# Kernel tuning notes

Hardware: AMD Instinct MI355X
Metric: run time of the kernel (lower is better)

## Reference

```python
import jax, jax.numpy as jnp
import numpy as np

TAU = 1.0
EPS_LN = 1e-5


def setup_inputs() -> dict:
    key = jax.random.key(0)
    ks = jax.random.split(key, 6)
    B, D, C, E, H = 32768, 768, 474, 3, 128
    x = jax.random.normal(ks[0], (B, D), dtype=jnp.float32)
    # pre-sampled uniform -> gumbel noise happens in reference; here store standard
    # gumbel noise directly (equivalent distribution to -log(-log(U)))
    u = jax.random.uniform(ks[1], (B, E), dtype=jnp.float32)
    gumbel_noise = -jnp.log(-jnp.log(u + 1e-20) + 1e-20)
    sel_w1 = jax.random.normal(ks[2], (D, H), dtype=jnp.float32) * (1.0 / np.sqrt(D))
    sel_b1 = jnp.zeros((H,), dtype=jnp.float32)
    sel_w2 = jax.random.normal(ks[3], (H, E), dtype=jnp.float32) * (1.0 / np.sqrt(H))
    sel_b2 = jnp.zeros((E,), dtype=jnp.float32)
    ln_gamma = jnp.ones((E, D), dtype=jnp.float32)
    ln_beta = jnp.zeros((E, D), dtype=jnp.float32)
    head_w = jax.random.normal(ks[4], (E, D, C), dtype=jnp.float32) * (1.0 / np.sqrt(D))
    head_b = jnp.zeros((E, C), dtype=jnp.float32)
    return {"x": x, "gumbel_noise": gumbel_noise, "sel_w1": sel_w1, "sel_b1": sel_b1,
            "sel_w2": sel_w2, "sel_b2": sel_b2, "ln_gamma": ln_gamma, "ln_beta": ln_beta,
            "head_w": head_w, "head_b": head_b}


def reference(x, gumbel_noise, sel_w1, sel_b1, sel_w2, sel_b2,
              ln_gamma, ln_beta, head_w, head_b):
    # selector MLP: Linear(768,128) -> ReLU -> Linear(128,3)
    h = jax.nn.relu(x @ sel_w1 + sel_b1)
    logits = h @ sel_w2 + sel_b2                       # [B, 3]

    # hard gumbel-softmax with straight-through estimator
    y = jax.nn.softmax((logits + gumbel_noise) / TAU, axis=-1)
    y_hard = jax.nn.one_hot(jnp.argmax(y, axis=-1), y.shape[-1], dtype=y.dtype)
    selection = jax.lax.stop_gradient(y_hard - y) + y  # [B, 3]

    # 3 expert heads: LayerNorm(768) -> Linear(768,474); dropout is identity (eval)
    mu = jnp.mean(x, axis=-1, keepdims=True)
    var = jnp.mean((x - mu) ** 2, axis=-1, keepdims=True)
    xn = (x - mu) * jax.lax.rsqrt(var + EPS_LN)        # [B, D]
    xs = xn[:, None, :] * ln_gamma[None] + ln_beta[None]   # [B, 3, D]
    outputs = jnp.einsum('bed,edc->bec', xs, head_w) + head_b  # [B, 3, C]

    # mask-and-sum combine
    return jnp.sum(outputs * selection[:, :, None], axis=1)    # [B, C]
```

## Files before the change

### kernel.cpp

```cpp
#include <hip/hip_runtime.h>
#include <hip/hip_bf16.h>
#include <math.h>

#define NB 32768
#define ND 768
#define NC 474
#define NCP 512
#define NE 3
#define NH 128
#define GAP_THR 0.035f
#define XB_OFF 4194304ull

typedef short v8s __attribute__((ext_vector_type(8)));
typedef float v4f __attribute__((ext_vector_type(4)));
typedef unsigned long long u64;

#define GLD16(gp, lp) __builtin_amdgcn_global_load_lds( \
    (const __attribute__((address_space(1))) void*)(gp), \
    (__attribute__((address_space(3))) void*)(lp), 16, 0, 0)

static __device__ __forceinline__ short f2bf(float f) {
    __hip_bfloat16 h = __float2bfloat16(f);
    return *reinterpret_cast<short*>(&h);
}

static __device__ __forceinline__ void vmwait(int n) {
    switch (n) {
    case 0:  asm volatile("s_waitcnt vmcnt(0)"  ::: "memory"); break;
    case 3:  asm volatile("s_waitcnt vmcnt(3)"  ::: "memory"); break;
    case 6:  asm volatile("s_waitcnt vmcnt(6)"  ::: "memory"); break;
    default: asm volatile("s_waitcnt vmcnt(10)" ::: "memory"); break;
    }
}

__global__ __launch_bounds__(256) void ln_convert(
    const float* __restrict__ x, float2* __restrict__ murs,
    short* __restrict__ xb)
{
    const int t = threadIdx.x;
    const int row = blockIdx.x * 16 + (t >> 4);
    const int q = t & 15;
    const float* xr = x + (size_t)row * ND;
    short* xo = xb + (size_t)row * ND;
    float4 v[12];
    #pragma unroll
    for (int i = 0; i < 12; ++i)
        v[i] = *(const float4*)(xr + (i * 16 + q) * 4);
    float s1 = 0.f, s2 = 0.f;
    #pragma unroll
    for (int i = 0; i < 12; ++i) {
        s1 += v[i].x + v[i].y + v[i].z + v[i].w;
        s2 += v[i].x*v[i].x + v[i].y*v[i].y + v[i].z*v[i].z + v[i].w*v[i].w;
    }
    #pragma unroll
    for (int i = 0; i < 12; ++i) {
        short4 o;
        o.x = f2bf(v[i].x); o.y = f2bf(v[i].y);
        o.z = f2bf(v[i].z); o.w = f2bf(v[i].w);
        *(short4*)(xo + (i * 16 + q) * 4) = o;
    }
    s1 += __shfl_xor(s1, 1); s2 += __shfl_xor(s2, 1);
    s1 += __shfl_xor(s1, 2); s2 += __shfl_xor(s2, 2);
    s1 += __shfl_xor(s1, 4); s2 += __shfl_xor(s2, 4);
    s1 += __shfl_xor(s1, 8); s2 += __shfl_xor(s2, 8);
    if (q == 0) {
        const float mu = s1 * (1.f / 768.f);
        const float var = s2 * (1.f / 768.f) - mu * mu;
        murs[row] = make_float2(mu, rsqrtf(var + 1e-5f));
    }
}

__global__ __launch_bounds__(256) void prep_kernel(
    const float* __restrict__ hw, const float* __restrict__ gamma,
    const float* __restrict__ beta, const float* __restrict__ w1,
    const float* __restrict__ hb,
    short* __restrict__ hwbT, short* __restrict__ w1bT,
    float* __restrict__ hbias, float* __restrict__ csumv)
{
    __shared__ float T[32][72];
    __shared__ float U[32][72];
    const int t = threadIdx.x;
    const int id = blockIdx.x;
    const float* src; short* dst; int stride, ncs; int e = 0, cc, kc;
    bool is_exp = (id < 576);
    if (is_exp) {
        e = id / 192; const int r2 = id % 192; cc = r2 / 24; kc = r2 % 24;
        src = hw + (size_t)e * ND * NC; stride = NC; ncs = NC;
        dst = hwbT + (size_t)e * NCP * ND;
    } else {
        const int j = id - 576; cc = j / 24; kc = j % 24;
        src = w1; stride = NH; ncs = NH; dst = w1bT;
    }
    const int c0 = cc * 64, k0 = kc * 32;
    {
        const int kl = t >> 3, c8 = (t & 7) * 8;
        const float g  = is_exp ? gamma[e * ND + k0 + kl] : 1.f;
        const float bb = is_exp ? beta[e * ND + k0 + kl]  : 0.f;
        #pragma unroll
        for (int j = 0; j < 8; ++j) {
            const int cg = c0 + c8 + j;
            const float v = (cg < ncs) ? src[(size_t)(k0 + kl) * stride + cg] : 0.f;
            T[kl][c8 + j] = v * g;
            U[kl][c8 + j] = v * bb;
        }
    }
    __syncthreads();
    {
        const int cl = t >> 2, q = t & 3;
        const int cg = c0 + cl;
        const int sp = q ^ ((cg >> 1) & 3);
        union { short s[8]; int4 v; } u;
        #pragma unroll
        for (int j = 0; j < 8; ++j) u.s[j] = f2bf(T[q * 8 + j][cl]);
        *(int4*)(dst + (size_t)cg * ND + k0 + sp * 8) = u.v;
    }
    if (is_exp && t < 64) {
        float sg = 0.f, sb = 0.f;
        #pragma unroll 8
        for (int k = 0; k < 32; ++k) {
            sg += T[k][t];
            sb += U[k][t];
        }
        const int c = c0 + t;
        if (kc == 0 && c < NC) sb += hb[e * NC + c];
        atomicAdd(&csumv[e * NCP + c], sg);
        atomicAdd(&hbias[e * NCP + c], sb);
    }
}

__global__ __launch_bounds__(256, 3) void selector_kernel(
    const short* __restrict__ xb, const float* __restrict__ gum,
    const short* __restrict__ w1bT, const float* __restrict__ b1,
    const float* __restrict__ w2, const float* __restrict__ b2,
    u64* __restrict__ counts,
    int* __restrict__ rowlist, int* __restrict__ redolist)
{
    __shared__ __align__(16) short As[3][2048];
    __shared__ __align__(16) short Bs[3][4096];
    __shared__ float wpart[4][64][3];
    __shared__ float b1s[NH], w2s[NH * 3];

    const int t = threadIdx.x;
    const int row0 = blockIdx.x * 64;
    const int w = t >> 6, l = t & 63;
    const int g = l >> 4, lm = l & 15;
    const int sr = t >> 2, sq = t & 3;

    if (t < NH) {
        b1s[t] = b1[t];
        w2s[t*3+0] = w2[t*3+0]; w2s[t*3+1] = w2[t*3+1]; w2s[t*3+2] = w2[t*3+2];
    }

    const int aslot = sq ^ ((sr >> 1) & 3);
    const short* axsrc = xb + (size_t)(row0 + sr) * ND + aslot * 8;
    const short* bsrc0 = w1bT + (size_t)(w * 32 +  0 + (l >> 2)) * ND + (l & 3) * 8;
    const short* bsrc1 = w1bT + (size_t)(w * 32 + 16 + (l >> 2)) * ND + (l & 3) * 8;
    const int aoff  = __builtin_amdgcn_readfirstlane(w * 512);
    const int boff0 = __builtin_amdgcn_readfirstlane((w * 32 +  0) * 32);
    const int boff1 = __builtin_amdgcn_readfirstlane((w * 32 + 16) * 32);

    v4f acc[4][2];
    #pragma unroll
    for (int i = 0; i < 4; ++i) { acc[i][0] = (v4f)(0.f); acc[i][1] = (v4f)(0.f); }

    __syncthreads();

    #pragma unroll
    for (int s = 0; s < 2; ++s) {
        GLD16(axsrc + s * 32, &As[s][0] + aoff);
        GLD16(bsrc0 + s * 32, &Bs[s][0] + boff0);
        GLD16(bsrc1 + s * 32, &Bs[s][0] + boff1);
    }

    #pragma unroll
    for (int ks = 0; ks < 24; ++ks) {
        const int cur = ks % 3;
        __builtin_amdgcn_s_barrier();
        __builtin_amdgcn_sched_barrier(0);
        if (ks < 22) {
            const int nxt = (ks + 2) % 3;
            GLD16(axsrc + (ks + 2) * 32, &As[nxt][0] + aoff);
            GLD16(bsrc0 + (ks + 2) * 32, &Bs[nxt][0] + boff0);
            GLD16(bsrc1 + (ks + 2) * 32, &Bs[nxt][0] + boff1);
            vmwait(6);
        } else {
            vmwait((23 - ks) * 3);
        }
        __builtin_amdgcn_sched_barrier(0);
        __builtin_amdgcn_s_barrier();

        v8s af[4];
        #pragma unroll
        for (int mf = 0; mf < 4; ++mf) {
            const int row = mf * 16 + lm;
            af[mf] = *(const v8s*)&As[cur][row * 32 + (g ^ ((lm >> 1) & 3)) * 8];
        }
        #pragma unroll
        for (int nf = 0; nf < 2; ++nf) {
            const int cl = w * 32 + nf * 16 + lm;
            const v8s bv = *(const v8s*)&Bs[cur][cl * 32 + (g ^ ((lm >> 1) & 3)) * 8];
            #pragma unroll
            for (int mf = 0; mf < 4; ++mf)
                acc[mf][nf] = __builtin_amdgcn_mfma_f32_16x16x32_bf16(
                    af[mf], bv, acc[mf][nf], 0, 0, 0);
        }
        asm volatile("s_waitcnt lgkmcnt(0)" ::: "memory");
        __builtin_amdgcn_sched_barrier(0);
    }

    #pragma unroll
    for (int mf = 0; mf < 4; ++mf) {
        float p[4][3] = {};
        #pragma unroll
        for (int nf = 0; nf < 2; ++nf) {
            const int cl = w * 32 + nf * 16 + lm;
            const float bb = b1s[cl];
            const float wa = w2s[cl*3], wb = w2s[cl*3+1], wc = w2s[cl*3+2];
            #pragma unroll
            for (int r = 0; r < 4; ++r) {
                const float h = fmaxf(acc[mf][nf][r] + bb, 0.f);
                p[r][0] = fmaf(h, wa, p[r][0]);
                p[r][1] = fmaf(h, wb, p[r][1]);
                p[r][2] = fmaf(h, wc, p[r][2]);
            }
        }
        #pragma unroll
        for (int m = 1; m < 16; m <<= 1)
            #pragma unroll
            for (int r = 0; r < 4; ++r) {
                p[r][0] += __shfl_xor(p[r][0], m);
                p[r][1] += __shfl_xor(p[r][1], m);
                p[r][2] += __shfl_xor(p[r][2], m);
            }
        if (lm == 0) {
            #pragma unroll
            for (int r = 0; r < 4; ++r) {
                const int row = mf * 16 + g * 4 + r;
                wpart[w][row][0] = p[r][0];
                wpart[w][row][1] = p[r][1];
                wpart[w][row][2] = p[r][2];
            }
        }
    }
    __syncthreads();

    if (t < 64) {
        const int grow = row0 + l;
        const float z0 = wpart[0][l][0] + wpart[1][l][0] + wpart[2][l][0]
                       + wpart[3][l][0] + b2[0] + gum[grow*3+0];
        const float z1 = wpart[0][l][1] + wpart[1][l][1] + wpart[2][l][1]
                       + wpart[3][l][1] + b2[1] + gum[grow*3+1];
        const float z2 = wpart[0][l][2] + wpart[1][l][2] + wpart[2][l][2]
                       + wpart[3][l][2] + b2[2] + gum[grow*3+2];
        int be = 0; float best = z0;
        if (z1 > best) { best = z1; be = 1; }
        if (z2 > best) { best = z2; be = 2; }
        const float second = (be==0) ? fmaxf(z1,z2) : (be==1) ? fmaxf(z0,z2) : fmaxf(z0,z1);
        if (best - second < GAP_THR) be = 3;

        const u64 m0 = __ballot(be == 0);
        const u64 m1 = __ballot(be == 1);
        const u64 m2 = __ballot(be == 2);
        const u64 m3 = __ballot(be == 3);
        u64 old = 0;
        if (l == 0) {
            const u64 add = (u64)__popcll(m0)
                          | ((u64)__popcll(m1) << 16)
                          | ((u64)__popcll(m2) << 32)
                          | ((u64)__popcll(m3) << 48);
            old = atomicAdd(counts, add);
        }
        const int blo = __shfl((int)(old & 0xFFFFFFFFull), 0);
        const int bhi = __shfl((int)(old >> 32), 0);
        old = ((u64)(unsigned)bhi << 32) | (u64)(unsigned)blo;
        const u64 mym = (be == 0) ? m0 : (be == 1) ? m1 : (be == 2) ? m2 : m3;
        const u64 below = (l == 63) ? 0x7FFFFFFFFFFFFFFFull : ((1ull << l) - 1ull);
        const int rank = __popcll(mym & below);
        const int base = (int)((old >> (16 * be)) & 0xFFFFull);
        const int idx = base + rank;
        if (be < 3) {
            if ((unsigned)idx < NB) rowlist[be * NB + idx] = grow;
        } else {
            if ((unsigned)idx < NB) redolist[idx] = grow;
        }
    }
}

__global__ __launch_bounds__(128) void redo_kernel(
    const float* __restrict__ x, const float* __restrict__ gum,
    const float* __restrict__ w1, const float* __restrict__ b1,
    const float* __restrict__ w2, const float* __restrict__ b2,
    u64* __restrict__ counts, int* __restrict__ rowlist,
    const int* __restrict__ redolist)
{
    const int t = threadIdx.x;
    int n = (int)((*counts >> 48) & 0xFFFFull);
    if (n > NB) n = NB;
    __shared__ float xs[ND];
    __shared__ double red[2][3];
    for (int i = blockIdx.x; i < n; i += gridDim.x) {
        const int row = redolist[i];
        {
            const float4* xp = (const float4*)(x + (size_t)row * ND);
            float4* xsv = (float4*)xs;
            xsv[t] = xp[t];
            if (t < 64) xsv[128 + t] = xp[128 + t];
        }
        __syncthreads();
        double h0 = 0.0, h1 = 0.0, h2 = 0.0, h3 = 0.0;
        double h4 = 0.0, h5 = 0.0, h6 = 0.0, h7 = 0.0;
        #pragma unroll 2
        for (int k = 0; k < ND; k += 8) {
            const float w0 = w1[(size_t)(k+0) * NH + t];
            const float w1v = w1[(size_t)(k+1) * NH + t];
            const float w2v = w1[(size_t)(k+2) * NH + t];
            const float w3 = w1[(size_t)(k+3) * NH + t];
            const float w4 = w1[(size_t)(k+4) * NH + t];
            const float w5 = w1[(size_t)(k+5) * NH + t];
            const float w6 = w1[(size_t)(k+6) * NH + t];
            const float w7 = w1[(size_t)(k+7) * NH + t];
            h0 = fma((double)xs[k+0], (double)w0, h0);
            h1 = fma((double)xs[k+1], (double)w1v, h1);
            h2 = fma((double)xs[k+2], (double)w2v, h2);
            h3 = fma((double)xs[k+3], (double)w3, h3);
            h4 = fma((double)xs[k+4], (double)w4, h4);
            h5 = fma((double)xs[k+5], (double)w5, h5);
            h6 = fma((double)xs[k+6], (double)w6, h6);
            h7 = fma((double)xs[k+7], (double)w7, h7);
        }
        double h = (((h0 + h1) + (h2 + h3)) + ((h4 + h5) + (h6 + h7)))
                 + (double)b1[t];
        h = h > 0.0 ? h : 0.0;
        double p0 = h * (double)w2[t * 3 + 0];
        double p1 = h * (double)w2[t * 3 + 1];
        double p2 = h * (double)w2[t * 3 + 2];
        #pragma unroll
        for (int m = 32; m >= 1; m >>= 1) {
            p0 += __shfl_xor(p0, m);
            p1 += __shfl_xor(p1, m);
            p2 += __shfl_xor(p2, m);
        }
        if ((t & 63) == 0) {
            red[t >> 6][0] = p0; red[t >> 6][1] = p1; red[t >> 6][2] = p2;
        }
        __syncthreads();
        if (t == 0) {
            double best = 0.0; int be = 0;
            #pragma unroll
            for (int e = 0; e < NE; ++e) {
                const double z = red[0][e] + red[1][e] + (double)b2[e]
                               + (double)gum[(size_t)row * 3 + e];
                if (e == 0 || z > best) { best = z; be = e; }
            }
            const u64 old = atomicAdd(counts, 1ull << (16 * be));
            const int pos = (int)((old >> (16 * be)) & 0xFFFFull);
            if ((unsigned)pos < NB) rowlist[be * NB + pos] = row;
        }
        __syncthreads();
    }
}

__global__ __launch_bounds__(256, 3) void head_kernel(
    const short* __restrict__ xb, const float2* __restrict__ murs,
    const short* __restrict__ hwbT, const float* __restrict__ hbias,
    const float* __restrict__ csumv,
    const u64* __restrict__ counts, const int* __restrict__ rowlist,
    float* __restrict__ out)
{
    const int e = blockIdx.z;
    int cnt = (int)((*counts >> (16 * e)) & 0xFFFFull);
    if (cnt > NB) cnt = NB;
    const int rc0 = blockIdx.y * 64;
    if (rc0 >= cnt) return;
    const int n0 = blockIdx.x * 256;

    __shared__ __align__(16) short As[2][64 * 32];
    __shared__ __align__(16) short Bs[2][256 * 32];
    __shared__ float hbs[256], css[256], rs_s[64], rm_s[64];
    __shared__ int rows_s[64];

    const int t = threadIdx.x;
    const int w = t >> 6, l = t & 63;
    const int g = l >> 4, lm = l & 15;
    const int sr = t >> 2, sq = t & 3;

    if (t < 64) {
        const int ri = rc0 + t;
        int rr = (ri < cnt) ? rowlist[e * NB + ri] : -1;
        if (rr >= NB) rr = -1;
        rows_s[t] = rr;
        const float2 mr = (rr >= 0) ? murs[rr] : make_float2(0.f, 0.f);
        rs_s[t] = mr.y;
        rm_s[t] = mr.y * mr.x;
    }
    hbs[t] = (n0 + t < NC) ? hbias[e * NCP + n0 + t] : 0.f;
    css[t] = (n0 + t < NC) ? csumv[e * NCP + n0 + t] : 0.f;

    const int ridx = rc0 + sr;
    int arow = (ridx < cnt) ? rowlist[e * NB + ridx] : 0;
    if ((unsigned)arow >= NB) arow = 0;
    const int aslot = sq ^ ((sr >> 1) & 3);
    const short* axsrc = xb + (size_t)arow * ND + aslot * 8;
    const short* hwe = hwbT + (size_t)e * NCP * ND + (size_t)n0 * ND;

    v4f acc[4][4];
    #pragma unroll
    for (int i = 0; i < 4; ++i)
        #pragma unroll
        for (int j = 0; j < 4; ++j) acc[i][j] = (v4f)(0.f);

    {
        const int aoff = __builtin_amdgcn_readfirstlane(w * 512);
        GLD16(axsrc, &As[0][0] + aoff);
    }
    #pragma unroll
    for (int i = 0; i < 4; ++i) {
        const int crow = w * 64 + i * 16 + (l >> 2);
        const int off = __builtin_amdgcn_readfirstlane((w * 64 + i * 16) * 32);
        GLD16(hwe + (size_t)crow * ND + (l & 3) * 8, &Bs[0][0] + off);
    }
    __syncthreads();

    #pragma unroll 2
    for (int ks = 0; ks < 24; ++ks) {
        const int cur = ks & 1;
        const int nxt = cur ^ 1;
        if (ks < 23) {
            const int kn = ks + 1;
            const int aoff = __builtin_amdgcn_readfirstlane(nxt * 2048 + w * 512);
            GLD16(axsrc + kn * 32, &As[0][0] + aoff);
            #pragma unroll
            for (int i = 0; i < 4; ++i) {
                const int crow = w * 64 + i * 16 + (l >> 2);
                const int off = __builtin_amdgcn_readfirstlane((w * 64 + i * 16) * 32);
                GLD16(hwe + (size_t)crow * ND + kn * 32 + (l & 3) * 8,
                      &Bs[nxt][0] + off);
            }
        }
        v8s af[4];
        #pragma unroll
        for (int mf = 0; mf < 4; ++mf) {
            const int row = mf * 16 + lm;
            af[mf] = *(const v8s*)&As[cur][row * 32 + (g ^ ((lm >> 1) & 3)) * 8];
        }
        #pragma unroll
        for (int nf = 0; nf < 4; ++nf) {
            const int cl = w * 64 + nf * 16 + lm;
            const v8s bv = *(const v8s*)&Bs[cur][cl * 32 + (g ^ ((lm >> 1) & 3)) * 8];
            #pragma unroll
            for (int mf = 0; mf < 4; ++mf)
                acc[mf][nf] = __builtin_amdgcn_mfma_f32_16x16x32_bf16(
                    af[mf], bv, acc[mf][nf], 0, 0, 0);
        }
        __syncthreads();
    }

    #pragma unroll
    for (int mf = 0; mf < 4; ++mf) {
        #pragma unroll
        for (int r = 0; r < 4; ++r) {
            const int rl = mf * 16 + g * 4 + r;
            const int orow = rows_s[rl];
            if (orow < 0) continue;
            const float rs = rs_s[rl], rm = rm_s[rl];
            float* op = out + (size_t)orow * NC;
            #pragma unroll
            for (int nf = 0; nf < 4; ++nf) {
                const int cl = w * 64 + nf * 16 + lm;
                const int c = n0 + cl;
                if (c < NC)
                    op[c] = acc[mf][nf][r] * rs - rm * css[cl] + hbs[cl];
            }
        }
    }
}

extern "C" void kernel_launch(void* const* d_in, const int* in_sizes, int n_in,
                              void* d_out, int out_size, void* d_ws, size_t ws_size,
                              hipStream_t stream) {
    const float* x     = (const float*)d_in[0];
    const float* gum   = (const float*)d_in[1];
    const float* w1    = (const float*)d_in[2];
    const float* b1    = (const float*)d_in[3];
    const float* w2    = (const float*)d_in[4];
    const float* b2    = (const float*)d_in[5];
    const float* gamma = (const float*)d_in[6];
    const float* beta  = (const float*)d_in[7];
    const float* hw    = (const float*)d_in[8];
    const float* hb    = (const float*)d_in[9];
    float* out = (float*)d_out;

    char* ws = (char*)d_ws;
    u64*    counts   = (u64*)ws;
    float2* murs     = (float2*)(ws + 256);
    int*    rowlist  = (int*)(ws + 262400);
    int*    redolist = (int*)(ws + 655616);
    float*  hbias    = (float*)(ws + 786688);
    float*  csumv    = (float*)(ws + 792832);
    short*  w1bT     = (short*)(ws + 798976);
    short*  hwbT     = (short*)(ws + 995584);
    short*  xbg      = (short*)(ws + XB_OFF);

    hipMemsetAsync(counts, 0, 16, stream);
    hipMemsetAsync(hbias, 0, 12288, stream);
    ln_convert<<<NB / 16, 256, 0, stream>>>(x, murs, xbg);
    prep_kernel<<<624, 256, 0, stream>>>(hw, gamma, beta, w1, hb,
                                         hwbT, w1bT, hbias, csumv);
    selector_kernel<<<NB / 64, 256, 0, stream>>>(xbg, gum, w1bT, b1, w2, b2,
                                                 counts, rowlist, redolist);
    redo_kernel<<<1024, 128, 0, stream>>>(x, gum, w1, b1, w2, b2,
                                          counts, rowlist, redolist);
    head_kernel<<<dim3(2, NB / 64, NE), 256, 0, stream>>>(
        xbg, murs, hwbT, hbias, csumv, counts, rowlist, out);
}
```

Before: 153.5 us.

## Halve selector row tile and deepen head-kernel A-operand pipeline with split barriers

```diff
diff --git a/kernel.cpp b/kernel.cpp
--- a/kernel.cpp
+++ b/kernel.cpp
@@ -28,6 +28,7 @@
     switch (n) {
     case 0:  asm volatile("s_waitcnt vmcnt(0)"  ::: "memory"); break;
     case 3:  asm volatile("s_waitcnt vmcnt(3)"  ::: "memory"); break;
+    case 5:  asm volatile("s_waitcnt vmcnt(5)"  ::: "memory"); break;
     case 6:  asm volatile("s_waitcnt vmcnt(6)"  ::: "memory"); break;
     default: asm volatile("s_waitcnt vmcnt(10)" ::: "memory"); break;
     }
@@ -128,40 +129,41 @@
     }
 }
 
-__global__ __launch_bounds__(256, 3) void selector_kernel(
+__global__ __launch_bounds__(256, 4) void selector_kernel(
     const short* __restrict__ xb, const float* __restrict__ gum,
     const short* __restrict__ w1bT, const float* __restrict__ b1,
     const float* __restrict__ w2, const float* __restrict__ b2,
     u64* __restrict__ counts,
     int* __restrict__ rowlist, int* __restrict__ redolist)
 {
-    __shared__ __align__(16) short As[3][2048];
+    __shared__ __align__(16) short As[3][1024];
     __shared__ __align__(16) short Bs[3][4096];
-    __shared__ float wpart[4][64][3];
+    __shared__ float wpart[4][32][3];
     __shared__ float b1s[NH], w2s[NH * 3];
 
     const int t = threadIdx.x;
-    const int row0 = blockIdx.x * 64;
+    const int row0 = blockIdx.x * 32;
     const int w = t >> 6, l = t & 63;
     const int g = l >> 4, lm = l & 15;
-    const int sr = t >> 2, sq = t & 3;
 
     if (t < NH) {
         b1s[t] = b1[t];
         w2s[t*3+0] = w2[t*3+0]; w2s[t*3+1] = w2[t*3+1]; w2s[t*3+2] = w2[t*3+2];
     }
 
+    const int sr = (w & 1) * 16 + (l >> 2);
+    const int sq = l & 3;
     const int aslot = sq ^ ((sr >> 1) & 3);
     const short* axsrc = xb + (size_t)(row0 + sr) * ND + aslot * 8;
     const short* bsrc0 = w1bT + (size_t)(w * 32 +  0 + (l >> 2)) * ND + (l & 3) * 8;
     const short* bsrc1 = w1bT + (size_t)(w * 32 + 16 + (l >> 2)) * ND + (l & 3) * 8;
-    const int aoff  = __builtin_amdgcn_readfirstlane(w * 512);
+    const int aoff  = __builtin_amdgcn_readfirstlane((w & 1) * 512);
     const int boff0 = __builtin_amdgcn_readfirstlane((w * 32 +  0) * 32);
     const int boff1 = __builtin_amdgcn_readfirstlane((w * 32 + 16) * 32);
 
-    v4f acc[4][2];
-    #pragma unroll
-    for (int i = 0; i < 4; ++i) { acc[i][0] = (v4f)(0.f); acc[i][1] = (v4f)(0.f); }
+    v4f acc[2][2];
+    #pragma unroll
+    for (int i = 0; i < 2; ++i) { acc[i][0] = (v4f)(0.f); acc[i][1] = (v4f)(0.f); }
 
     __syncthreads();
 
@@ -189,9 +191,9 @@
         __builtin_amdgcn_sched_barrier(0);
         __builtin_amdgcn_s_barrier();
 
-        v8s af[4];
-        #pragma unroll
-        for (int mf = 0; mf < 4; ++mf) {
+        v8s af[2];
+        #pragma unroll
+        for (int mf = 0; mf < 2; ++mf) {
             const int row = mf * 16 + lm;
             af[mf] = *(const v8s*)&As[cur][row * 32 + (g ^ ((lm >> 1) & 3)) * 8];
         }
@@ -200,7 +202,7 @@
             const int cl = w * 32 + nf * 16 + lm;
             const v8s bv = *(const v8s*)&Bs[cur][cl * 32 + (g ^ ((lm >> 1) & 3)) * 8];
             #pragma unroll
-            for (int mf = 0; mf < 4; ++mf)
+            for (int mf = 0; mf < 2; ++mf)
                 acc[mf][nf] = __builtin_amdgcn_mfma_f32_16x16x32_bf16(
                     af[mf], bv, acc[mf][nf], 0, 0, 0);
         }
@@ -209,7 +211,7 @@
     }
 
     #pragma unroll
-    for (int mf = 0; mf < 4; ++mf) {
+    for (int mf = 0; mf < 2; ++mf) {
         float p[4][3] = {};
         #pragma unroll
         for (int nf = 0; nf < 2; ++nf) {
@@ -244,7 +246,7 @@
     }
     __syncthreads();
 
-    if (t < 64) {
+    if (t < 32) {
         const int grow = row0 + l;
         const float z0 = wpart[0][l][0] + wpart[1][l][0] + wpart[2][l][0]
                        + wpart[3][l][0] + b2[0] + gum[grow*3+0];
@@ -274,7 +276,7 @@
         const int bhi = __shfl((int)(old >> 32), 0);
         old = ((u64)(unsigned)bhi << 32) | (u64)(unsigned)blo;
         const u64 mym = (be == 0) ? m0 : (be == 1) ? m1 : (be == 2) ? m2 : m3;
-        const u64 below = (l == 63) ? 0x7FFFFFFFFFFFFFFFull : ((1ull << l) - 1ull);
+        const u64 below = (1ull << l) - 1ull;
         const int rank = __popcll(mym & below);
         const int base = (int)((old >> (16 * be)) & 0xFFFFull);
         const int idx = base + rank;
@@ -374,8 +376,8 @@
     if (rc0 >= cnt) return;
     const int n0 = blockIdx.x * 256;
 
-    __shared__ __align__(16) short As[2][64 * 32];
-    __shared__ __align__(16) short Bs[2][256 * 32];
+    __shared__ __align__(16) short As[3][2048];
+    __shared__ __align__(16) short Bs[2][8192];
     __shared__ float hbs[256], css[256], rs_s[64], rm_s[64];
     __shared__ int rows_s[64];
 
@@ -402,6 +404,7 @@
     const int aslot = sq ^ ((sr >> 1) & 3);
     const short* axsrc = xb + (size_t)arow * ND + aslot * 8;
     const short* hwe = hwbT + (size_t)e * NCP * ND + (size_t)n0 * ND;
+    const int aoff = __builtin_amdgcn_readfirstlane(w * 512);
 
     v4f acc[4][4];
     #pragma unroll
@@ -409,50 +412,57 @@
         #pragma unroll
         for (int j = 0; j < 4; ++j) acc[i][j] = (v4f)(0.f);
 
-    {
-        const int aoff = __builtin_amdgcn_readfirstlane(w * 512);
-        GLD16(axsrc, &As[0][0] + aoff);
-    }
     #pragma unroll
     for (int i = 0; i < 4; ++i) {
         const int crow = w * 64 + i * 16 + (l >> 2);
         const int off = __builtin_amdgcn_readfirstlane((w * 64 + i * 16) * 32);
         GLD16(hwe + (size_t)crow * ND + (l & 3) * 8, &Bs[0][0] + off);
     }
+    GLD16(axsrc,      &As[0][0] + aoff);
+    GLD16(axsrc + 32, &As[1][0] + aoff);
     __syncthreads();
 
-    #pragma unroll 2
+    #pragma unroll
     for (int ks = 0; ks < 24; ++ks) {
-        const int cur = ks & 1;
-        const int nxt = cur ^ 1;
+        const int cur3 = ks % 3;
+        const int curb = ks & 1;
+        __builtin_amdgcn_s_barrier();
+        __builtin_amdgcn_sched_barrier(0);
         if (ks < 23) {
-            const int kn = ks + 1;
-            const int aoff = __builtin_amdgcn_readfirstlane(nxt * 2048 + w * 512);
-            GLD16(axsrc + kn * 32, &As[0][0] + aoff);
             #pragma unroll
             for (int i = 0; i < 4; ++i) {
                 const int crow = w * 64 + i * 16 + (l >> 2);
                 const int off = __builtin_amdgcn_readfirstlane((w * 64 + i * 16) * 32);
-                GLD16(hwe + (size_t)crow * ND + kn * 32 + (l & 3) * 8,
-                      &Bs[nxt][0] + off);
+                GLD16(hwe + (size_t)crow * ND + (ks + 1) * 32 + (l & 3) * 8,
+                      &Bs[(ks + 1) & 1][0] + off);
             }
         }
+        if (ks < 22) {
+            GLD16(axsrc + (ks + 2) * 32, &As[(ks + 2) % 3][0] + aoff);
+        }
+        if (ks < 22)      vmwait(6);
+        else if (ks == 22) vmwait(5);
+        else               vmwait(0);
+        __builtin_amdgcn_sched_barrier(0);
+        __builtin_amdgcn_s_barrier();
+
         v8s af[4];
         #pragma unroll
         for (int mf = 0; mf < 4; ++mf) {
             const int row = mf * 16 + lm;
-            af[mf] = *(const v8s*)&As[cur][row * 32 + (g ^ ((lm >> 1) & 3)) * 8];
+            af[mf] = *(const v8s*)&As[cur3][row * 32 + (g ^ ((lm >> 1) & 3)) * 8];
         }
         #pragma unroll
         for (int nf = 0; nf < 4; ++nf) {
             const int cl = w * 64 + nf * 16 + lm;
-            const v8s bv = *(const v8s*)&Bs[cur][cl * 32 + (g ^ ((lm >> 1) & 3)) * 8];
+            const v8s bv = *(const v8s*)&Bs[curb][cl * 32 + (g ^ ((lm >> 1) & 3)) * 8];
             #pragma unroll
             for (int mf = 0; mf < 4; ++mf)
                 acc[mf][nf] = __builtin_amdgcn_mfma_f32_16x16x32_bf16(
                     af[mf], bv, acc[mf][nf], 0, 0, 0);
         }
-        __syncthreads();
+        asm volatile("s_waitcnt lgkmcnt(0)" ::: "memory");
+        __builtin_amdgcn_sched_barrier(0);
     }
 
     #pragma unroll
@@ -506,7 +516,7 @@
     ln_convert<<<NB / 16, 256, 0, stream>>>(x, murs, xbg);
     prep_kernel<<<624, 256, 0, stream>>>(hw, gamma, beta, w1, hb,
                                          hwbT, w1bT, hbias, csumv);
-    selector_kernel<<<NB / 64, 256, 0, stream>>>(xbg, gum, w1bT, b1, w2, b2,
+    selector_kernel<<<NB / 32, 256, 0, stream>>>(xbg, gum, w1bT, b1, w2, b2,
                                                  counts, rowlist, redolist);
     redo_kernel<<<1024, 128, 0, stream>>>(x, gum, w1, b1, w2, b2,
                                           counts, rowlist, redolist);
```

New measurement: 160.0 us. +4.2%, slower.
